# Performance work log

Measured on AMD Instinct MI355X. Metric: run time of the kernel, lower is better.

The kernel has to match this reference:

```python
import jax, jax.numpy as jnp
import numpy as np

N = 100000
IN_CH = 128
OUT_CH = 32
HEADS = 4
E = 1600000
NEG_SLOPE = 0.2  # PyG GATConv default negative_slope


def setup_inputs() -> dict:
    key = jax.random.key(0)
    k_x, k_e, k_w, k_as, k_ad, k_b = jax.random.split(key, 6)
    x = jax.random.normal(k_x, (N, IN_CH), dtype=jnp.float32)
    edge_index = jax.random.randint(k_e, (2, E), 0, N, dtype=jnp.int64)
    # Glorot-style scale for linear weight, small normals for attention vectors
    W = jax.random.normal(k_w, (IN_CH, HEADS * OUT_CH), dtype=jnp.float32) * (1.0 / np.sqrt(IN_CH))
    att_src = jax.random.normal(k_as, (1, HEADS, OUT_CH), dtype=jnp.float32) * 0.1
    att_dst = jax.random.normal(k_ad, (1, HEADS, OUT_CH), dtype=jnp.float32) * 0.1
    bias = jnp.zeros((HEADS * OUT_CH,), dtype=jnp.float32)
    return {"x": x, "edge_index": edge_index, "W": W,
            "att_src": att_src, "att_dst": att_dst, "bias": bias}


def reference(x, edge_index, W, att_src, att_dst, bias):
    n = x.shape[0]
    # Linear transform: [N, H, C]
    xw = (x @ W).reshape(n, HEADS, OUT_CH)
    # Per-node attention logits: [N, H]
    a_src = (xw * att_src).sum(-1)
    a_dst = (xw * att_dst).sum(-1)
    # Add self-loops (PyG GATConv default add_self_loops=True)
    loop = jnp.arange(n, dtype=edge_index.dtype)
    src = jnp.concatenate([edge_index[0], loop])  # [E']
    dst = jnp.concatenate([edge_index[1], loop])  # [E']
    # Edge-wise attention logits + leaky relu: [E', H]
    alpha = jax.nn.leaky_relu(a_src[src] + a_dst[dst], NEG_SLOPE)
    # Segment softmax over edges grouped by destination node
    amax = jax.ops.segment_max(alpha, dst, num_segments=n)
    alpha = jnp.exp(alpha - amax[dst])
    denom = jax.ops.segment_sum(alpha, dst, num_segments=n)
    alpha = alpha / (denom[dst] + 1e-16)
    # Weighted scatter-aggregate of source features: [N, H, C]
    msg = xw[src] * alpha[:, :, None]
    out = jax.ops.segment_sum(msg, dst, num_segments=n)
    out = out.reshape(n, HEADS * OUT_CH) + bias
    return jax.nn.elu(out)
```

## Files before the change

kernel.cpp:

```cpp
#include <hip/hip_runtime.h>
#include <cmath>


#define LOG2E 1.44269504088896340736f

typedef float f32x2 __attribute__((ext_vector_type(2)));
typedef float f32x4 __attribute__((ext_vector_type(4)));

__device__ __forceinline__ float fast_exp2(float x) {
#if __has_builtin(__builtin_amdgcn_exp2f)
  return __builtin_amdgcn_exp2f(x);
#else
  return exp2f(x);
#endif
}

__device__ __forceinline__ unsigned bf16_rne(float f) {
  unsigned u = __float_as_uint(f);
  return (u + 0x7fffu + ((u >> 16) & 1u)) >> 16;
}
__device__ __forceinline__ float bf_lo(unsigned v) {
  return __uint_as_float(v << 16);
}
__device__ __forceinline__ float bf_hi(unsigned v) {
  return __uint_as_float(v & 0xffff0000u);
}

__device__ __forceinline__ int blockInclScan(int v, int tid, int* lds) {
  int lane = tid & 63;
  int wid = tid >> 6;
#pragma unroll
  for (int off = 1; off < 64; off <<= 1) {
    int t = __shfl_up(v, off);
    if (lane >= off) v += t;
  }
  if (lane == 63) lds[wid] = v;
  __syncthreads();
  int add = 0;
  for (int i = 0; i < wid; ++i) add += lds[i];
  v += add;
  __syncthreads();
  return v;
}

#define CHUNK 4096
#define MAXE 2560

__global__ __launch_bounds__(256) void k_hist(const int* __restrict__ ei, int E,
                                              int EL, int NB2, int NBLK,
                                              int* __restrict__ bh,
                                              int* __restrict__ btot) {
  __shared__ int lh[1792];
  int tid = threadIdx.x;
  for (int b = tid; b < NB2; b += 256) lh[b] = 0;
  __syncthreads();
  int base_e = blockIdx.x * CHUNK;
#pragma unroll
  for (int j = 0; j < CHUNK / 256; ++j) {
    int e = base_e + j * 256 + tid;
    if (e < EL) {
      int dst = (e < E) ? ei[E + e] : (e - E);
      atomicAdd(&lh[dst >> 6], 1);
    }
  }
  __syncthreads();
  for (int b = tid; b < NB2; b += 256) {
    int c = lh[b];
    bh[(size_t)b * NBLK + blockIdx.x] = c;
    if (c) atomicAdd(&btot[b], c);
  }
}

__global__ __launch_bounds__(256) void p2c_brow(int* __restrict__ bh,
                                                const int* __restrict__ btot,
                                                int* __restrict__ bbase,
                                                int NB2, int NBLK) {
  __shared__ int lds[4];
  __shared__ int ctot;
  __shared__ int red[256];
  int b = blockIdx.x;
  int tid = threadIdx.x;
  int part = 0;
  for (int j = tid; j < b; j += 256) part += btot[j];
  red[tid] = part;
  __syncthreads();
  for (int st = 128; st > 0; st >>= 1) {
    if (tid < st) red[tid] += red[tid + st];
    __syncthreads();
  }
  int base = red[0];
  if (tid == 0) bbase[b] = base;
  __syncthreads();
  int v0 = (tid < NBLK) ? bh[(size_t)b * NBLK + tid] : 0;
  int incl0 = blockInclScan(v0, tid, lds);
  if (tid < NBLK) bh[(size_t)b * NBLK + tid] = base + incl0 - v0;
  if (tid == 255) ctot = incl0;
  __syncthreads();
  int base1 = base + ctot;
  int j = 256 + tid;
  int v1 = (j < NBLK) ? bh[(size_t)b * NBLK + j] : 0;
  int incl1 = blockInclScan(v1, tid, lds);
  if (j < NBLK) bh[(size_t)b * NBLK + j] = base1 + incl1 - v1;
}

__global__ __launch_bounds__(256) void k_fusedB(
    const float* __restrict__ x, const float* __restrict__ Wm,
    const float* __restrict__ att_src, const float* __restrict__ att_dst,
    unsigned* __restrict__ xwb, float* __restrict__ a_src,
    float* __restrict__ a_dst, int N, int GB,
    const int* __restrict__ ei, int E, int EL, int NB2, int NBLK,
    const int* __restrict__ bh, unsigned* __restrict__ tmp) {
  __shared__ __align__(16) char sm[33280];
  const int tid = threadIdx.x;

  if ((int)blockIdx.x >= GB) {
    int blk = blockIdx.x - GB;
    int* lc = (int*)sm;
    for (int b = tid; b < NB2; b += 256) lc[b] = bh[(size_t)b * NBLK + blk];
    __syncthreads();
    int base_e = blk * CHUNK;
#pragma unroll
    for (int j = 0; j < CHUNK / 256; ++j) {
      int e = base_e + j * 256 + tid;
      if (e < EL) {
        int src, dst;
        if (e < E) {
          src = ei[e];
          dst = ei[E + e];
        } else {
          src = e - E;
          dst = e - E;
        }
        int pos = atomicAdd(&lc[dst >> 6], 1);
        tmp[pos] = ((unsigned)(dst & 63) << 17) | (unsigned)src;
      }
    }
    return;
  }

  float (*xs_t)[132] = (float(*)[132])sm;
  float (*Wl)[128] = (float(*)[128])(sm + 16896);
  const int tx = tid & 15;
  const int ty = tid >> 4;
  const int row0 = blockIdx.x * 128;

  float acc[8][8];
#pragma unroll
  for (int r = 0; r < 8; ++r)
#pragma unroll
    for (int c = 0; c < 8; ++c) acc[r][c] = 0.f;

  for (int kc = 0; kc < 4; ++kc) {
    __syncthreads();
#pragma unroll
    for (int j = 0; j < 4; ++j) {
      int f = tid + j * 256;
      int r = f >> 3, k4 = f & 7;
      int row = row0 + r;
      float4 v = make_float4(0.f, 0.f, 0.f, 0.f);
      if (row < N) v = *(const float4*)&x[(size_t)row * 128 + kc * 32 + k4 * 4];
      xs_t[k4 * 4 + 0][r] = v.x;
      xs_t[k4 * 4 + 1][r] = v.y;
      xs_t[k4 * 4 + 2][r] = v.z;
      xs_t[k4 * 4 + 3][r] = v.w;
    }
#pragma unroll
    for (int j = 0; j < 4; ++j) {
      int f = tid + j * 256;
      int kr = f >> 5, c4 = f & 31;
      *(float4*)&Wl[kr][c4 * 4] =
          *(const float4*)&Wm[(size_t)(kc * 32 + kr) * 128 + c4 * 4];
    }
    __syncthreads();
#pragma unroll 4
    for (int k = 0; k < 32; ++k) {
      float wv[8], xv[8];
      *(float4*)&wv[0] = *(const float4*)&Wl[k][tx * 8];
      *(float4*)&wv[4] = *(const float4*)&Wl[k][tx * 8 + 4];
      *(float4*)&xv[0] = *(const float4*)&xs_t[k][ty * 8];
      *(float4*)&xv[4] = *(const float4*)&xs_t[k][ty * 8 + 4];
#pragma unroll
      for (int r = 0; r < 8; ++r)
#pragma unroll
        for (int c = 0; c < 8; ++c) acc[r][c] = fmaf(xv[r], wv[c], acc[r][c]);
    }
  }

  float att_s[8], att_d[8];
#pragma unroll
  for (int c = 0; c < 8; ++c) {
    att_s[c] = att_src[tx * 8 + c];
    att_d[c] = att_dst[tx * 8 + c];
  }

#pragma unroll
  for (int r = 0; r < 8; ++r) {
    int row = row0 + ty * 8 + r;
    bool ok = row < N;
    float vs = 0.f, vd = 0.f;
#pragma unroll
    for (int c = 0; c < 8; ++c) {
      vs += acc[r][c] * att_s[c];
      vd += acc[r][c] * att_d[c];
    }
    vs += __shfl_xor(vs, 1);
    vs += __shfl_xor(vs, 2);
    vd += __shfl_xor(vd, 1);
    vd += __shfl_xor(vd, 2);
    if (ok) {
      uint4 pk;
      pk.x = bf16_rne(acc[r][0]) | (bf16_rne(acc[r][1]) << 16);
      pk.y = bf16_rne(acc[r][2]) | (bf16_rne(acc[r][3]) << 16);
      pk.z = bf16_rne(acc[r][4]) | (bf16_rne(acc[r][5]) << 16);
      pk.w = bf16_rne(acc[r][6]) | (bf16_rne(acc[r][7]) << 16);
      *(uint4*)&xwb[(size_t)row * 64 + tx * 4] = pk;
      if ((tx & 3) == 0) {
        a_src[row * 4 + (tx >> 2)] = vs * LOG2E;
        a_dst[row * 4 + (tx >> 2)] = vd * LOG2E;
      }
    }
  }
}

__global__ __launch_bounds__(256) void k_bagg(
    const unsigned* __restrict__ tmp, const int* __restrict__ bbase,
    const int* __restrict__ btot, const float* __restrict__ asrc,
    const float* __restrict__ adst, const unsigned* __restrict__ xwb,
    const float* __restrict__ bias, float* __restrict__ out, int N) {
  __shared__ unsigned sorted[MAXE];
  __shared__ int deg[64];
  __shared__ int startd[64];
  __shared__ int cur[64];
  const int bid = blockIdx.x;
  const int tid = threadIdx.x;
  const int beg = bbase[bid];
  const int cnt = btot[bid];
  if (tid < 64) deg[tid] = 0;
  __syncthreads();
  for (int k = tid; k < cnt; k += 256) {
    unsigned w = tmp[beg + k];
    atomicAdd(&deg[w >> 17], 1);
  }
  __syncthreads();
  if (tid < 64) {
    int v = deg[tid];
    int incl = v;
#pragma unroll
    for (int off = 1; off < 64; off <<= 1) {
      int t = __shfl_up(incl, off);
      if (tid >= off) incl += t;
    }
    int excl = incl - v;
    startd[tid] = excl;
    cur[tid] = excl;
  }
  __syncthreads();
  for (int k = tid; k < cnt; k += 256) {
    unsigned w = tmp[beg + k];
    int pos = atomicAdd(&cur[w >> 17], 1);
    if (pos < MAXE) sorted[pos] = w;
  }
  __syncthreads();
  const int wv = tid >> 6;
  const int lane = tid & 63;
  const int half = lane >> 5;
  const int l5 = lane & 31;
  const int h = l5 >> 3;
  const unsigned* xr = xwb + l5 * 2;
  const float4 bv = *(const float4*)&bias[l5 * 4];

  for (int j = 0; j < 16; ++j) {
    int dl = wv + 4 * j;
    int gdst = bid * 64 + dl;
    if (gdst >= N) break;
    int sd = startd[dl];
    int ed = min(sd + deg[dl], MAXE);
    float ad = adst[gdst * 4 + h];

    float sA = 0.f, sB = 0.f;
    float a0 = 0.f, a1 = 0.f, a2 = 0.f, a3 = 0.f;
    float b0 = 0.f, b1 = 0.f, b2 = 0.f, b3 = 0.f;
    int i = sd + half;
    for (; i + 6 < ed; i += 8) {
      unsigned wA = sorted[i], wB = sorted[i + 2];
      unsigned wC = sorted[i + 4], wD = sorted[i + 6];
      int eA = wA & 0x1FFFF, eB = wB & 0x1FFFF;
      int eC = wC & 0x1FFFF, eD = wD & 0x1FFFF;
      float tA = asrc[eA * 4 + h] + ad;
      float tB = asrc[eB * 4 + h] + ad;
      float tC = asrc[eC * 4 + h] + ad;
      float tD = asrc[eD * 4 + h] + ad;
      uint2 vA = *(const uint2*)(xr + (size_t)eA * 64);
      uint2 vB = *(const uint2*)(xr + (size_t)eB * 64);
      uint2 vC = *(const uint2*)(xr + (size_t)eC * 64);
      uint2 vD = *(const uint2*)(xr + (size_t)eD * 64);
      float pA = fast_exp2(fmaxf(tA, 0.2f * tA));
      float pB = fast_exp2(fmaxf(tB, 0.2f * tB));
      float pC = fast_exp2(fmaxf(tC, 0.2f * tC));
      float pD = fast_exp2(fmaxf(tD, 0.2f * tD));
      sA += pA + pC;
      sB += pB + pD;
      a0 = fmaf(pA, bf_lo(vA.x), a0);
      a1 = fmaf(pA, bf_hi(vA.x), a1);
      a2 = fmaf(pA, bf_lo(vA.y), a2);
      a3 = fmaf(pA, bf_hi(vA.y), a3);
      b0 = fmaf(pB, bf_lo(vB.x), b0);
      b1 = fmaf(pB, bf_hi(vB.x), b1);
      b2 = fmaf(pB, bf_lo(vB.y), b2);
      b3 = fmaf(pB, bf_hi(vB.y), b3);
      a0 = fmaf(pC, bf_lo(vC.x), a0);
      a1 = fmaf(pC, bf_hi(vC.x), a1);
      a2 = fmaf(pC, bf_lo(vC.y), a2);
      a3 = fmaf(pC, bf_hi(vC.y), a3);
      b0 = fmaf(pD, bf_lo(vD.x), b0);
      b1 = fmaf(pD, bf_hi(vD.x), b1);
      b2 = fmaf(pD, bf_lo(vD.y), b2);
      b3 = fmaf(pD, bf_hi(vD.y), b3);
    }
    for (; i < ed; i += 2) {
      unsigned wA = sorted[i];
      int eA = wA & 0x1FFFF;
      float tA = asrc[eA * 4 + h] + ad;
      uint2 vA = *(const uint2*)(xr + (size_t)eA * 64);
      float pA = fast_exp2(fmaxf(tA, 0.2f * tA));
      sA += pA;
      a0 = fmaf(pA, bf_lo(vA.x), a0);
      a1 = fmaf(pA, bf_hi(vA.x), a1);
      a2 = fmaf(pA, bf_lo(vA.y), a2);
      a3 = fmaf(pA, bf_hi(vA.y), a3);
    }
    float s = sA + sB;
    a0 += b0;
    a1 += b1;
    a2 += b2;
    a3 += b3;
    s += __shfl_xor(s, 32);
    a0 += __shfl_xor(a0, 32);
    a1 += __shfl_xor(a1, 32);
    a2 += __shfl_xor(a2, 32);
    a3 += __shfl_xor(a3, 32);

    if (half == 0) {
      float inv = 1.f / s;
      float o0 = fmaf(a0, inv, bv.x);
      float o1 = fmaf(a1, inv, bv.y);
      float o2 = fmaf(a2, inv, bv.z);
      float o3 = fmaf(a3, inv, bv.w);
      o0 = o0 > 0.f ? o0 : fast_exp2(o0 * LOG2E) - 1.f;
      o1 = o1 > 0.f ? o1 : fast_exp2(o1 * LOG2E) - 1.f;
      o2 = o2 > 0.f ? o2 : fast_exp2(o2 * LOG2E) - 1.f;
      o3 = o3 > 0.f ? o3 : fast_exp2(o3 * LOG2E) - 1.f;
      f32x4 o = {o0, o1, o2, o3};
      __builtin_nontemporal_store(o, (f32x4*)&out[(size_t)gdst * 128 + l5 * 4]);
    }
  }
}

extern "C" void kernel_launch(void* const* d_in, const int* in_sizes, int n_in,
                              void* d_out, int out_size, void* d_ws, size_t ws_size,
                              hipStream_t stream) {
  const float* x = (const float*)d_in[0];
  const int* ei = (const int*)d_in[1];
  const float* Wm = (const float*)d_in[2];
  const float* att_src = (const float*)d_in[3];
  const float* att_dst = (const float*)d_in[4];
  const float* bias = (const float*)d_in[5];
  float* out = (float*)d_out;

  const int N = in_sizes[0] / 128;
  const int E = in_sizes[1] / 2;
  const int EL = E + N;
  const int NB2 = (N + 63) >> 6;
  const int NBLK = (EL + CHUNK - 1) / CHUNK;
  const int GB = (N + 127) / 128;

  size_t off = 0;
  auto carve = [&](size_t bytes) -> void* {
    void* p = (char*)d_ws + off;
    off += (bytes + 255) & ~(size_t)255;
    return p;
  };
  unsigned* xwb = (unsigned*)carve((size_t)N * 64 * 4);
  float* a_src = (float*)carve((size_t)N * 4 * 4);
  float* a_dst = (float*)carve((size_t)N * 4 * 4);
  unsigned* tmp = (unsigned*)carve((size_t)EL * 4);
  int* bh = (int*)carve((size_t)NB2 * NBLK * 4);
  int* btot = (int*)carve((size_t)NB2 * 4);
  int* bbase = (int*)carve((size_t)NB2 * 4);

  (void)hipMemsetAsync(btot, 0, (size_t)NB2 * 4, stream);

  k_hist<<<NBLK, 256, 0, stream>>>(ei, E, EL, NB2, NBLK, bh, btot);
  p2c_brow<<<NB2, 256, 0, stream>>>(bh, btot, bbase, NB2, NBLK);
  k_fusedB<<<GB + NBLK, 256, 0, stream>>>(x, Wm, att_src, att_dst, xwb, a_src,
                                          a_dst, N, GB, ei, E, EL, NB2, NBLK,
                                          bh, tmp);
  k_bagg<<<NB2, 256, 0, stream>>>(tmp, bbase, btot, a_src, a_dst, xwb,
                                  bias, out, N);
}
```

Before: 178.8 us.

## Use bf16 MFMA for node linear transform with folded attention columns

Replaces the FP32 register-tiled GEMM for x@W with bf16 MFMA 16x16x32 instructions, staging W as bf16 in LDS. The attention projections are folded into the GEMM as extra output columns: W·att_src and W·att_dst are precomputed by an extra block in the histogram kernel, so a_src/a_dst come out of a ninth MFMA tile. This targets the FP32 FMA cost of the dense stage. In exchange x is rounded to bf16 before multiplication and the attention logits are computed in bf16, which lowers precision.

```diff
diff --git a/kernel.cpp b/kernel.cpp
--- a/kernel.cpp
+++ b/kernel.cpp
@@ -6,6 +6,8 @@
 
 typedef float f32x2 __attribute__((ext_vector_type(2)));
 typedef float f32x4 __attribute__((ext_vector_type(4)));
+typedef unsigned u32x4 __attribute__((ext_vector_type(4)));
+typedef short bf16x8 __attribute__((ext_vector_type(8)));
 
 __device__ __forceinline__ float fast_exp2(float x) {
 #if __has_builtin(__builtin_amdgcn_exp2f)
@@ -49,7 +51,30 @@
 __global__ __launch_bounds__(256) void k_hist(const int* __restrict__ ei, int E,
                                               int EL, int NB2, int NBLK,
                                               int* __restrict__ bh,
-                                              int* __restrict__ btot) {
+                                              int* __restrict__ btot,
+                                              const float* __restrict__ Wm,
+                                              const float* __restrict__ att_src,
+                                              const float* __restrict__ att_dst,
+                                              unsigned short* __restrict__ u_bf) {
+  if ((int)blockIdx.x == NBLK) {
+    int k = threadIdx.x;
+    if (k < 128) {
+      const float* wr = Wm + (size_t)k * 128;
+      float s[8] = {0.f, 0.f, 0.f, 0.f, 0.f, 0.f, 0.f, 0.f};
+      for (int c = 0; c < 32; ++c) {
+#pragma unroll
+        for (int h = 0; h < 4; ++h) {
+          float wv = wr[h * 32 + c];
+          s[h] = fmaf(wv, att_src[h * 32 + c], s[h]);
+          s[4 + h] = fmaf(wv, att_dst[h * 32 + c], s[4 + h]);
+        }
+      }
+#pragma unroll
+      for (int j = 0; j < 8; ++j)
+        u_bf[k * 8 + j] = (unsigned short)bf16_rne(s[j]);
+    }
+    return;
+  }
   __shared__ int lh[1792];
   int tid = threadIdx.x;
   for (int b = tid; b < NB2; b += 256) lh[b] = 0;
@@ -105,16 +130,15 @@
 
 __global__ __launch_bounds__(256) void k_fusedB(
     const float* __restrict__ x, const float* __restrict__ Wm,
-    const float* __restrict__ att_src, const float* __restrict__ att_dst,
-    unsigned* __restrict__ xwb, float* __restrict__ a_src,
-    float* __restrict__ a_dst, int N, int GB,
+    const unsigned short* __restrict__ u_bf, unsigned* __restrict__ xwb,
+    float* __restrict__ a_src, float* __restrict__ a_dst, int N, int GB2,
     const int* __restrict__ ei, int E, int EL, int NB2, int NBLK,
     const int* __restrict__ bh, unsigned* __restrict__ tmp) {
-  __shared__ __align__(16) char sm[33280];
+  __shared__ __align__(16) char sm[36864];
   const int tid = threadIdx.x;
 
-  if ((int)blockIdx.x >= GB) {
-    int blk = blockIdx.x - GB;
+  if ((int)blockIdx.x >= GB2) {
+    int blk = blockIdx.x - GB2;
     int* lc = (int*)sm;
     for (int b = tid; b < NB2; b += 256) lc[b] = bh[(size_t)b * NBLK + blk];
     __syncthreads();
@@ -138,86 +162,84 @@
     return;
   }
 
-  float (*xs_t)[132] = (float(*)[132])sm;
-  float (*Wl)[128] = (float(*)[128])(sm + 16896);
-  const int tx = tid & 15;
-  const int ty = tid >> 4;
-  const int row0 = blockIdx.x * 128;
-
-  float acc[8][8];
-#pragma unroll
-  for (int r = 0; r < 8; ++r)
-#pragma unroll
-    for (int c = 0; c < 8; ++c) acc[r][c] = 0.f;
-
-  for (int kc = 0; kc < 4; ++kc) {
-    __syncthreads();
-#pragma unroll
-    for (int j = 0; j < 4; ++j) {
-      int f = tid + j * 256;
-      int r = f >> 3, k4 = f & 7;
-      int row = row0 + r;
-      float4 v = make_float4(0.f, 0.f, 0.f, 0.f);
-      if (row < N) v = *(const float4*)&x[(size_t)row * 128 + kc * 32 + k4 * 4];
-      xs_t[k4 * 4 + 0][r] = v.x;
-      xs_t[k4 * 4 + 1][r] = v.y;
-      xs_t[k4 * 4 + 2][r] = v.z;
-      xs_t[k4 * 4 + 3][r] = v.w;
-    }
-#pragma unroll
-    for (int j = 0; j < 4; ++j) {
-      int f = tid + j * 256;
-      int kr = f >> 5, c4 = f & 31;
-      *(float4*)&Wl[kr][c4 * 4] =
-          *(const float4*)&Wm[(size_t)(kc * 32 + kr) * 128 + c4 * 4];
-    }
-    __syncthreads();
-#pragma unroll 4
-    for (int k = 0; k < 32; ++k) {
-      float wv[8], xv[8];
-      *(float4*)&wv[0] = *(const float4*)&Wl[k][tx * 8];
-      *(float4*)&wv[4] = *(const float4*)&Wl[k][tx * 8 + 4];
-      *(float4*)&xv[0] = *(const float4*)&xs_t[k][ty * 8];
-      *(float4*)&xv[4] = *(const float4*)&xs_t[k][ty * 8 + 4];
-#pragma unroll
-      for (int r = 0; r < 8; ++r)
-#pragma unroll
-        for (int c = 0; c < 8; ++c) acc[r][c] = fmaf(xv[r], wv[c], acc[r][c]);
-    }
-  }
-
-  float att_s[8], att_d[8];
-#pragma unroll
-  for (int c = 0; c < 8; ++c) {
-    att_s[c] = att_src[tx * 8 + c];
-    att_d[c] = att_dst[tx * 8 + c];
-  }
-
-#pragma unroll
-  for (int r = 0; r < 8; ++r) {
-    int row = row0 + ty * 8 + r;
-    bool ok = row < N;
-    float vs = 0.f, vd = 0.f;
-#pragma unroll
-    for (int c = 0; c < 8; ++c) {
-      vs += acc[r][c] * att_s[c];
-      vd += acc[r][c] * att_d[c];
-    }
-    vs += __shfl_xor(vs, 1);
-    vs += __shfl_xor(vs, 2);
-    vd += __shfl_xor(vd, 1);
-    vd += __shfl_xor(vd, 2);
-    if (ok) {
-      uint4 pk;
-      pk.x = bf16_rne(acc[r][0]) | (bf16_rne(acc[r][1]) << 16);
-      pk.y = bf16_rne(acc[r][2]) | (bf16_rne(acc[r][3]) << 16);
-      pk.z = bf16_rne(acc[r][4]) | (bf16_rne(acc[r][5]) << 16);
-      pk.w = bf16_rne(acc[r][6]) | (bf16_rne(acc[r][7]) << 16);
-      *(uint4*)&xwb[(size_t)row * 64 + tx * 4] = pk;
-      if ((tx & 3) == 0) {
-        a_src[row * 4 + (tx >> 2)] = vs * LOG2E;
-        a_dst[row * 4 + (tx >> 2)] = vd * LOG2E;
+  short* Ws = (short*)sm;
+  {
+    int r = tid & 127;
+    int ch = tid >> 7;
+    int kk = r >> 5, g = (r >> 3) & 3, i = r & 7;
+    short* drow = Ws + ((kk * 4 + g) * 144) * 8 + i;
+    const float* srow = Wm + (size_t)r * 128 + ch * 64;
+#pragma unroll
+    for (int c4 = 0; c4 < 16; ++c4) {
+      float4 v = *(const float4*)&srow[c4 * 4];
+      int c0 = ch * 64 + c4 * 4;
+      drow[(c0 + 0) * 8] = (short)bf16_rne(v.x);
+      drow[(c0 + 1) * 8] = (short)bf16_rne(v.y);
+      drow[(c0 + 2) * 8] = (short)bf16_rne(v.z);
+      drow[(c0 + 3) * 8] = (short)bf16_rne(v.w);
+    }
+    if (tid < 128) {
+#pragma unroll
+      for (int j = 0; j < 8; ++j) drow[(128 + j) * 8] = (short)u_bf[r * 8 + j];
+#pragma unroll
+      for (int j = 8; j < 16; ++j) drow[(128 + j) * 8] = 0;
+    }
+  }
+  __syncthreads();
+
+  const int w = tid >> 6;
+  const int l = tid & 63;
+  const int lr = l & 15;
+  const int lg = l >> 4;
+  const int row0w = blockIdx.x * 64 + w * 16;
+  const int arow = row0w + lr;
+
+  f32x4 acc[9];
+#pragma unroll
+  for (int t = 0; t < 9; ++t) acc[t] = (f32x4){0.f, 0.f, 0.f, 0.f};
+
+  const float* xrow = x + (size_t)arow * 128 + lg * 8;
+#pragma unroll
+  for (int kk = 0; kk < 4; ++kk) {
+    unsigned p0 = 0, p1 = 0, p2 = 0, p3 = 0;
+    if (arow < N) {
+      float4 f0 = *(const float4*)&xrow[kk * 32];
+      float4 f1 = *(const float4*)&xrow[kk * 32 + 4];
+      p0 = bf16_rne(f0.x) | (bf16_rne(f0.y) << 16);
+      p1 = bf16_rne(f0.z) | (bf16_rne(f0.w) << 16);
+      p2 = bf16_rne(f1.x) | (bf16_rne(f1.y) << 16);
+      p3 = bf16_rne(f1.z) | (bf16_rne(f1.w) << 16);
+    }
+    u32x4 ap = {p0, p1, p2, p3};
+    bf16x8 af = __builtin_bit_cast(bf16x8, ap);
+    const short* wsbase = Ws + ((kk * 4 + lg) * 144 + lr) * 8;
+#pragma unroll
+    for (int t = 0; t < 9; ++t) {
+      bf16x8 bf = *(const bf16x8*)(wsbase + t * 128);
+      acc[t] = __builtin_amdgcn_mfma_f32_16x16x32_bf16(af, bf, acc[t], 0, 0, 0);
+    }
+  }
+
+#pragma unroll
+  for (int t = 0; t < 8; ++t) {
+#pragma unroll
+    for (int i = 0; i < 4; ++i) {
+      float v = acc[t][i];
+      float vn = __shfl_xor(v, 1);
+      int row = row0w + 4 * lg + i;
+      if (!(l & 1) && row < N) {
+        unsigned pk = bf16_rne(v) | (bf16_rne(vn) << 16);
+        xwb[(size_t)row * 64 + 8 * t + (lr >> 1)] = pk;
       }
+    }
+  }
+#pragma unroll
+  for (int i = 0; i < 4; ++i) {
+    int row = row0w + 4 * lg + i;
+    if (lr < 8 && row < N) {
+      float v = acc[8][i] * LOG2E;
+      if (lr < 4) a_src[row * 4 + lr] = v;
+      else a_dst[row * 4 + lr - 4] = v;
     }
   }
 }
@@ -372,7 +394,7 @@
   const int EL = E + N;
   const int NB2 = (N + 63) >> 6;
   const int NBLK = (EL + CHUNK - 1) / CHUNK;
-  const int GB = (N + 127) / 128;
+  const int GB2 = (N + 63) / 64;
 
   size_t off = 0;
   auto carve = [&](size_t bytes) -> void* {
@@ -387,14 +409,15 @@
   int* bh = (int*)carve((size_t)NB2 * NBLK * 4);
   int* btot = (int*)carve((size_t)NB2 * 4);
   int* bbase = (int*)carve((size_t)NB2 * 4);
+  unsigned short* u_bf = (unsigned short*)carve(128 * 8 * 2);
 
   (void)hipMemsetAsync(btot, 0, (size_t)NB2 * 4, stream);
 
-  k_hist<<<NBLK, 256, 0, stream>>>(ei, E, EL, NB2, NBLK, bh, btot);
+  k_hist<<<NBLK + 1, 256, 0, stream>>>(ei, E, EL, NB2, NBLK, bh, btot, Wm,
+                                       att_src, att_dst, u_bf);
   p2c_brow<<<NB2, 256, 0, stream>>>(bh, btot, bbase, NB2, NBLK);
-  k_fusedB<<<GB + NBLK, 256, 0, stream>>>(x, Wm, att_src, att_dst, xwb, a_src,
-                                          a_dst, N, GB, ei, E, EL, NB2, NBLK,
-                                          bh, tmp);
+  k_fusedB<<<GB2 + NBLK, 256, 0, stream>>>(x, Wm, u_bf, xwb, a_src, a_dst, N,
+                                           GB2, ei, E, EL, NB2, NBLK, bh, tmp);
   k_bagg<<<NB2, 256, 0, stream>>>(tmp, bbase, btot, a_src, a_dst, xwb,
                                   bias, out, N);
 }
```

Result: faster. 164.1 us (-8.2%).
